# Kernel optimization log

Measured on AMD Instinct MI355X. Metric: run time of the kernel, lower is better.

The kernel has to match this reference:

```python
import jax, jax.numpy as jnp
import numpy as np

N_NODES = 50000
N_EDGES = 1000000
F_IN, HID, N_CLS, HEADS = 128, 16, 40, 8
NEG_SLOPE = 0.2


def setup_inputs() -> dict:
    key = jax.random.key(0)
    ks = jax.random.split(key, 12)
    x = jax.random.normal(ks[0], (N_NODES, F_IN), dtype=jnp.float32)
    edge_index = jax.random.randint(ks[1], (2, N_EDGES), 0, N_NODES, dtype=jnp.int32)
    s1 = 1.0 / np.sqrt(F_IN)
    s2 = 1.0 / np.sqrt(HID)
    return {
        "x": x,
        "edge_index": edge_index,
        # conv1: heads=8, out=HID, concat=False (mean over heads)
        "W1": jax.random.normal(ks[2], (F_IN, HEADS * HID), dtype=jnp.float32) * s1,
        "att_src1": jax.random.normal(ks[3], (HEADS, HID), dtype=jnp.float32) * s2,
        "att_dst1": jax.random.normal(ks[4], (HEADS, HID), dtype=jnp.float32) * s2,
        "b1": jnp.zeros((HID,), dtype=jnp.float32),
        # conv2: heads=1, out=N_CLS
        "W2": jax.random.normal(ks[5], (HID, N_CLS), dtype=jnp.float32) * s2,
        "att_src2": jax.random.normal(ks[6], (1, N_CLS), dtype=jnp.float32),
        "att_dst2": jax.random.normal(ks[7], (1, N_CLS), dtype=jnp.float32),
        "b2": jnp.zeros((N_CLS,), dtype=jnp.float32),
    }


def _gat_conv(x, src, dst, W, att_src, att_dst, num_nodes):
    """One GATConv (PyG semantics, eval mode). Returns [N, H, C]."""
    H, C = att_src.shape
    h = (x @ W).reshape(-1, H, C)                       # [N, H, C]
    a_s = (h * att_src[None]).sum(-1)                   # [N, H]
    a_d = (h * att_dst[None]).sum(-1)                   # [N, H]
    e = jax.nn.leaky_relu(a_s[src] + a_d[dst], NEG_SLOPE)  # [E, H]
    # segment softmax over edges grouped by destination node
    m = jax.ops.segment_max(e, dst, num_segments=num_nodes)     # [N, H]
    ex = jnp.exp(e - m[dst])
    denom = jax.ops.segment_sum(ex, dst, num_segments=num_nodes)
    alpha = ex / (denom[dst] + 1e-16)                   # [E, H]
    msg = h[src] * alpha[:, :, None]                    # [E, H, C]
    return jax.ops.segment_sum(msg, dst, num_segments=num_nodes)  # [N, H, C]


def reference(x, edge_index, W1, att_src1, att_dst1, b1, W2, att_src2, att_dst2, b2):
    n = x.shape[0]
    loops = jnp.arange(n, dtype=edge_index.dtype)
    src = jnp.concatenate([edge_index[0], loops])
    dst = jnp.concatenate([edge_index[1], loops])

    # conv1: concat=False -> mean over heads, then bias; then ELU
    h1 = _gat_conv(x, src, dst, W1, att_src1, att_dst1, n).mean(axis=1) + b1
    h1 = jax.nn.elu(h1)
    # dropout is identity in eval mode

    # conv2: heads=1, concat (trivial) -> squeeze head dim, add bias
    h2 = _gat_conv(h1, src, dst, W2, att_src2, att_dst2, n)[:, 0, :] + b2
    return jax.nn.log_softmax(h2, axis=1)
```

## Files before the change

kernel.cpp:

```cpp
#include <hip/hip_runtime.h>
#include <hip/hip_fp16.h>
#include <math.h>

#define N_NODES 50000
#define N_EDGES 1000000
#define F_IN 128
#define HID 16
#define N_CLS 40
#define HEADS 8
#define ET (N_EDGES + N_NODES)
#define XB ((N_NODES + 63) / 64)
#define NBK 196
#define NSB 256
#define ECH ((ET + NSB - 1) / NSB)

__device__ __forceinline__ void fma4(float4& acc, float s, const float4& v) {
  acc.x += s * v.x;
  acc.y += s * v.y;
  acc.z += s * v.z;
  acc.w += s * v.w;
}

__device__ __forceinline__ float dot4(float4 a, float4 b) {
  return a.x * b.x + a.y * b.y + a.z * b.z + a.w * b.w;
}

__device__ __forceinline__ unsigned encf(float f) {
  unsigned b = __float_as_uint(f);
  return (b & 0x80000000u) ? ~b : (b | 0x80000000u);
}
__device__ __forceinline__ float decf(unsigned k) {
  unsigned b = (k & 0x80000000u) ? (k ^ 0x80000000u) : ~k;
  return __uint_as_float(b);
}


__global__ __launch_bounds__(256, 4) void k_xform1(
    const float* __restrict__ x, const float* __restrict__ W1,
    const float* __restrict__ att_s, const float* __restrict__ att_d,
    __half* __restrict__ h1, float* __restrict__ as1, float* __restrict__ ad1,
    unsigned* __restrict__ enc1) {
  __shared__ float4 xlds[64 * 9];
  __shared__ float4 wlds[32 * 33];
  __shared__ unsigned encl[8];
  int t = threadIdx.x;
  if (t < 8) encl[t] = 0u;
  int tx = t & 15, ty = t >> 4;
  int base = blockIdx.x * 64;
  const float4* x4 = (const float4*)x;
  const float4* W4 = (const float4*)W1;

  float4 accA[4], accB[4];
#pragma unroll
  for (int n = 0; n < 4; n++) {
    accA[n] = {0.f, 0.f, 0.f, 0.f};
    accB[n] = {0.f, 0.f, 0.f, 0.f};
  }
  int n0 = ty * 4;

  for (int kb = 0; kb < 4; kb++) {
    __syncthreads();
    {
      int i = t;
      int n = i >> 3, q = i & 7;
      int gn = base + n;
      float4 v = {0.f, 0.f, 0.f, 0.f};
      if (gn < N_NODES) v = x4[(size_t)gn * 32 + kb * 8 + q];
      xlds[n * 9 + q] = v;
      i += 256;
      n = i >> 3; q = i & 7;
      gn = base + n;
      float4 v2 = {0.f, 0.f, 0.f, 0.f};
      if (gn < N_NODES) v2 = x4[(size_t)gn * 32 + kb * 8 + q];
      xlds[n * 9 + q] = v2;
    }
#pragma unroll
    for (int u = 0; u < 4; u++) {
      int i = t + u * 256;
      int r = i >> 5, q = i & 31;
      wlds[r * 33 + q] = W4[(size_t)(kb * 32 + r) * 32 + q];
    }
    __syncthreads();
#pragma unroll
    for (int kk = 0; kk < 8; kk++) {
      float4 xv0 = xlds[(n0 + 0) * 9 + kk];
      float4 xv1 = xlds[(n0 + 1) * 9 + kk];
      float4 xv2 = xlds[(n0 + 2) * 9 + kk];
      float4 xv3 = xlds[(n0 + 3) * 9 + kk];
#pragma unroll
      for (int j = 0; j < 4; j++) {
        float4 wA = wlds[(kk * 4 + j) * 33 + tx];
        float4 wB = wlds[(kk * 4 + j) * 33 + tx + 16];
        float s0 = (j == 0) ? xv0.x : (j == 1) ? xv0.y : (j == 2) ? xv0.z : xv0.w;
        float s1 = (j == 0) ? xv1.x : (j == 1) ? xv1.y : (j == 2) ? xv1.z : xv1.w;
        float s2 = (j == 0) ? xv2.x : (j == 1) ? xv2.y : (j == 2) ? xv2.z : xv2.w;
        float s3 = (j == 0) ? xv3.x : (j == 1) ? xv3.y : (j == 2) ? xv3.z : xv3.w;
        fma4(accA[0], s0, wA); fma4(accB[0], s0, wB);
        fma4(accA[1], s1, wA); fma4(accB[1], s1, wB);
        fma4(accA[2], s2, wA); fma4(accB[2], s2, wB);
        fma4(accA[3], s3, wA); fma4(accB[3], s3, wB);
      }
    }
  }

  int c4 = tx * 4;
  float4 asA = *(const float4*)(att_s + c4);
  float4 asB = *(const float4*)(att_s + 64 + c4);
  float4 adA = *(const float4*)(att_d + c4);
  float4 adB = *(const float4*)(att_d + 64 + c4);
  float mxA = -1e30f, mxB = -1e30f;
#pragma unroll
  for (int n = 0; n < 4; n++) {
    int gn = base + n0 + n;
    float psA = dot4(accA[n], asA);
    float psB = dot4(accB[n], asB);
    float pdA = dot4(accA[n], adA);
    float pdB = dot4(accB[n], adB);
    psA += __shfl_xor(psA, 1); psA += __shfl_xor(psA, 2);
    psB += __shfl_xor(psB, 1); psB += __shfl_xor(psB, 2);
    pdA += __shfl_xor(pdA, 1); pdA += __shfl_xor(pdA, 2);
    pdB += __shfl_xor(pdB, 1); pdB += __shfl_xor(pdB, 2);
    if (gn < N_NODES) {
      uint2 pkA, pkB;
      __half2* phA = (__half2*)&pkA;
      __half2* phB = (__half2*)&pkB;
      phA[0] = __floats2half2_rn(accA[n].x, accA[n].y);
      phA[1] = __floats2half2_rn(accA[n].z, accA[n].w);
      phB[0] = __floats2half2_rn(accB[n].x, accB[n].y);
      phB[1] = __floats2half2_rn(accB[n].z, accB[n].w);
      *(uint2*)(h1 + (size_t)gn * 128 + c4) = pkA;
      *(uint2*)(h1 + (size_t)gn * 128 + 64 + c4) = pkB;
      mxA = fmaxf(mxA, psA);
      mxB = fmaxf(mxB, psB);
      if ((tx & 3) == 0) {
        as1[gn * 8 + (tx >> 2)] = psA;
        as1[gn * 8 + 4 + (tx >> 2)] = psB;
        ad1[gn * 8 + (tx >> 2)] = pdA;
        ad1[gn * 8 + 4 + (tx >> 2)] = pdB;
      }
    }
  }
  if ((tx & 3) == 0) {
    atomicMax(&encl[tx >> 2], encf(mxA));
    atomicMax(&encl[4 + (tx >> 2)], encf(mxB));
  }
  __syncthreads();
  if (t < 8) atomicMax(&enc1[t], encl[t]);
}


__global__ __launch_bounds__(256) void k_rxA(const int* __restrict__ ei,
                                             int* __restrict__ bcnt) {
  __shared__ int cnt[NBK];
  int t = threadIdx.x, blk = blockIdx.x;
  if (t < NBK) cnt[t] = 0;
  __syncthreads();
  int lo = blk * ECH + t;
  int hi = min((blk + 1) * ECH, ET);
  for (int i = lo; i < hi; i += 256) {
    int d = (i < N_EDGES) ? ei[N_EDGES + i] : (i - N_EDGES);
    atomicAdd(&cnt[d >> 8], 1);
  }
  __syncthreads();
  if (t < NBK) bcnt[t * NSB + blk] = cnt[t];
}


__global__ __launch_bounds__(256) void k_rxScanB(const int* __restrict__ bcnt,
                                                 int* __restrict__ boffs,
                                                 int* __restrict__ btot) {
  __shared__ int s[256];
  int b = blockIdx.x, t = threadIdx.x;
  int v0 = bcnt[b * NSB + t];
  s[t] = v0;
  __syncthreads();
  for (int off = 1; off < 256; off <<= 1) {
    int v = (t >= off) ? s[t - off] : 0;
    __syncthreads();
    s[t] += v;
    __syncthreads();
  }
  boffs[b * NSB + t] = s[t] - v0;
  if (t == 255) btot[b] = s[255];
}


__global__ __launch_bounds__(256) void k_rxTot(const int* __restrict__ btot,
                                               int* __restrict__ bstart,
                                               int* __restrict__ start,
                                               const unsigned* __restrict__ enc1,
                                               float* __restrict__ fmax1) {
  __shared__ int s[256];
  int t = threadIdx.x;
  int v0 = (t < NBK) ? btot[t] : 0;
  s[t] = v0;
  __syncthreads();
  for (int off = 1; off < 256; off <<= 1) {
    int v = (t >= off) ? s[t - off] : 0;
    __syncthreads();
    s[t] += v;
    __syncthreads();
  }
  if (t < NBK) bstart[t] = s[t] - v0;
  if (t == 0) start[N_NODES] = ET;
  if (t < 8) fmax1[t] = decf(enc1[t]);
}


__global__ __launch_bounds__(256) void k_rxScat(const int* __restrict__ ei,
                                                const int* __restrict__ bstart,
                                                const int* __restrict__ boffs,
                                                int2* __restrict__ eb) {
  __shared__ int cur[NBK];
  int t = threadIdx.x, blk = blockIdx.x;
  if (t < NBK) cur[t] = bstart[t] + boffs[t * NSB + blk];
  __syncthreads();
  int lo = blk * ECH + t;
  int hi = min((blk + 1) * ECH, ET);
  for (int i = lo; i < hi; i += 256) {
    int s, d;
    if (i < N_EDGES) { s = ei[i]; d = ei[N_EDGES + i]; }
    else { s = i - N_EDGES; d = s; }
    int pos = atomicAdd(&cur[d >> 8], 1);
    eb[pos] = make_int2(s, d);
  }
}


__global__ __launch_bounds__(256) void k_rxB(const int2* __restrict__ eb,
                                             const int* __restrict__ bstart,
                                             int* __restrict__ start,
                                             int* __restrict__ esrc) {
  __shared__ int dcnt[256], lst[256], ssc[256];
  __shared__ int esl[8192];
  int t = threadIdx.x, b = blockIdx.x;
  int nlo = b * 256;
  int nn = min(256, N_NODES - nlo);
  int e0 = bstart[b];
  int e1 = (b == NBK - 1) ? ET : bstart[b + 1];
  int cnt = e1 - e0;
  dcnt[t] = 0;
  __syncthreads();
  for (int e = t; e < cnt; e += 256) atomicAdd(&dcnt[eb[e0 + e].y & 255], 1);
  __syncthreads();
  int v0 = dcnt[t];
  ssc[t] = v0;
  __syncthreads();
  for (int off = 1; off < 256; off <<= 1) {
    int v = (t >= off) ? ssc[t - off] : 0;
    __syncthreads();
    ssc[t] += v;
    __syncthreads();
  }
  lst[t] = ssc[t] - v0;
  if (t < nn) start[nlo + t] = e0 + lst[t];
  dcnt[t] = lst[t];
  __syncthreads();
  for (int e = t; e < cnt; e += 256) {
    int2 p = eb[e0 + e];
    int pos = atomicAdd(&dcnt[p.y & 255], 1);
    esl[pos] = p.x;
  }
  __syncthreads();
  for (int e = t; e < cnt; e += 256) esrc[e0 + e] = esl[e];
}


__global__ __launch_bounds__(256) void k_agg1(
    const __half* __restrict__ h1, const float* __restrict__ as1,
    const float* __restrict__ ad1, const int* __restrict__ start,
    const int* __restrict__ esrc, const float* __restrict__ b1,
    const float* __restrict__ W2, const float* __restrict__ att_s2,
    const float* __restrict__ att_d2, const float* __restrict__ fmax1,
    __half* __restrict__ h2, float* __restrict__ as2, float* __restrict__ ad2) {
  __shared__ __align__(16) __half2 p_t[4][4 * 164];
  __shared__ __align__(16) int s_off[4][4][20];
  __shared__ float w2s[16 * 40];
  int t = threadIdx.x;
  for (int i = t; i < 640; i += 256) w2s[i] = W2[i];
  __syncthreads();

  int wave = t >> 6, lane = t & 63;
  int g = lane >> 4, li = lane & 15;
  int d = blockIdx.x * 16 + wave * 4 + g;
  int s0 = start[d];
  int deg = start[d + 1] - s0;

  int dm = deg;
  dm = max(dm, __shfl_xor(dm, 16));
  dm = max(dm, __shfl_xor(dm, 32));

  float4 av0 = *(const float4*)(ad1 + d * 8);
  float4 av1 = *(const float4*)(ad1 + d * 8 + 4);
  float ad_[8] = {av0.x, av0.y, av0.z, av0.w, av1.x, av1.y, av1.z, av1.w};
  float c_[8];
#pragma unroll
  for (int h = 0; h < 8; h++) {
    float e = fmax1[h] + ad_[h];
    c_[h] = e > 0.f ? e : 0.2f * e;
  }

  float den = 0.f;
  float accf[8];
#pragma unroll
  for (int k = 0; k < 8; k++) accf[k] = 0.f;

  int hsel = li >> 1;
  const char* h1l = (const char*)(h1 + li * 8);
  __half2* ptw = &p_t[wave][g * 164];
  const int* so = &s_off[wave][g][0];

  for (int be = 0; be < dm; be += 16) {
    int cnt = deg - be;
    bool act = li < cnt;
    int s = 0;
    if (act) s = esrc[s0 + be + li];
    s_off[wave][g][li] = act ? (s << 8) : 0;
    float4 p0 = {0.f, 0.f, 0.f, 0.f}, p1 = {0.f, 0.f, 0.f, 0.f};
    if (act) {
      p0 = *(const float4*)(as1 + (size_t)s * 8);
      p1 = *(const float4*)(as1 + (size_t)s * 8 + 4);
    }
    float ev[8] = {p0.x, p0.y, p0.z, p0.w, p1.x, p1.y, p1.z, p1.w};
#pragma unroll
    for (int h = 0; h < 8; h++) {
      float v = ev[h] + ad_[h];
      v = v > 0.f ? v : 0.2f * v;
      float pv = act ? __expf(v - c_[h]) : 0.f;
      __half hp = __float2half(pv);
      ptw[h * 20 + li] = __half2{hp, hp};
    }
    asm volatile("s_waitcnt lgkmcnt(0)" ::: "memory");

    int cm = min(dm - be, 16);
    const __half2* pt = ptw + hsel * 20;
    __half2 a0 = __floats2half2_rn(0.f, 0.f);
    __half2 a1 = __floats2half2_rn(0.f, 0.f);
    __half2 a2 = __floats2half2_rn(0.f, 0.f);
    __half2 a3 = __floats2half2_rn(0.f, 0.f);
    for (int e = 0; e < cm; e += 8) {
      int4 s4 = *(const int4*)&so[e];
      int4 s8 = *(const int4*)&so[e + 4];
      uint4 pwA = *(const uint4*)&pt[e];
      uint4 pwB = *(const uint4*)&pt[e + 4];
      const __half2* ppA = (const __half2*)&pwA;
      const __half2* ppB = (const __half2*)&pwB;
      uint4 hA = *(const uint4*)(h1l + (unsigned)s4.x);
      uint4 hB = *(const uint4*)(h1l + (unsigned)s4.y);
      uint4 hC = *(const uint4*)(h1l + (unsigned)s4.z);
      uint4 hD = *(const uint4*)(h1l + (unsigned)s4.w);
      uint4 hE = *(const uint4*)(h1l + (unsigned)s8.x);
      uint4 hF = *(const uint4*)(h1l + (unsigned)s8.y);
      uint4 hG = *(const uint4*)(h1l + (unsigned)s8.z);
      uint4 hH = *(const uint4*)(h1l + (unsigned)s8.w);
      const __half2* vA = (const __half2*)&hA;
      const __half2* vB = (const __half2*)&hB;
      const __half2* vC = (const __half2*)&hC;
      const __half2* vD = (const __half2*)&hD;
      const __half2* vE = (const __half2*)&hE;
      const __half2* vF = (const __half2*)&hF;
      const __half2* vG = (const __half2*)&hG;
      const __half2* vH = (const __half2*)&hH;
      a0 = __hfma2(vA[0], ppA[0], a0); a1 = __hfma2(vA[1], ppA[0], a1);
      a2 = __hfma2(vA[2], ppA[0], a2); a3 = __hfma2(vA[3], ppA[0], a3);
      a0 = __hfma2(vB[0], ppA[1], a0); a1 = __hfma2(vB[1], ppA[1], a1);
      a2 = __hfma2(vB[2], ppA[1], a2); a3 = __hfma2(vB[3], ppA[1], a3);
      a0 = __hfma2(vC[0], ppA[2], a0); a1 = __hfma2(vC[1], ppA[2], a1);
      a2 = __hfma2(vC[2], ppA[2], a2); a3 = __hfma2(vC[3], ppA[2], a3);
      a0 = __hfma2(vD[0], ppA[3], a0); a1 = __hfma2(vD[1], ppA[3], a1);
      a2 = __hfma2(vD[2], ppA[3], a2); a3 = __hfma2(vD[3], ppA[3], a3);
      a0 = __hfma2(vE[0], ppB[0], a0); a1 = __hfma2(vE[1], ppB[0], a1);
      a2 = __hfma2(vE[2], ppB[0], a2); a3 = __hfma2(vE[3], ppB[0], a3);
      a0 = __hfma2(vF[0], ppB[1], a0); a1 = __hfma2(vF[1], ppB[1], a1);
      a2 = __hfma2(vF[2], ppB[1], a2); a3 = __hfma2(vF[3], ppB[1], a3);
      a0 = __hfma2(vG[0], ppB[2], a0); a1 = __hfma2(vG[1], ppB[2], a1);
      a2 = __hfma2(vG[2], ppB[2], a2); a3 = __hfma2(vG[3], ppB[2], a3);
      a0 = __hfma2(vH[0], ppB[3], a0); a1 = __hfma2(vH[1], ppB[3], a1);
      a2 = __hfma2(vH[2], ppB[3], a2); a3 = __hfma2(vH[3], ppB[3], a3);
      den += __low2float(ppA[0]) + __low2float(ppA[1]) +
             __low2float(ppA[2]) + __low2float(ppA[3]) +
             __low2float(ppB[0]) + __low2float(ppB[1]) +
             __low2float(ppB[2]) + __low2float(ppB[3]);
    }
    float2 f0 = __half22float2(a0), f1 = __half22float2(a1);
    float2 f2 = __half22float2(a2), f3 = __half22float2(a3);
    accf[0] += f0.x; accf[1] += f0.y; accf[2] += f1.x; accf[3] += f1.y;
    accf[4] += f2.x; accf[5] += f2.y; accf[6] += f3.x; accf[7] += f3.y;
    asm volatile("s_waitcnt lgkmcnt(0)" ::: "memory");
  }

  float sc = 0.125f / den;
#pragma unroll
  for (int k = 0; k < 8; k++) accf[k] *= sc;
#pragma unroll
  for (int off = 2; off <= 8; off <<= 1) {
#pragma unroll
    for (int k = 0; k < 8; k++) accf[k] += __shfl_xor(accf[k], off);
  }
  int jb = (li & 1) * 8;
  float4 b1a = *(const float4*)(b1 + jb);
  float4 b1b = *(const float4*)(b1 + jb + 4);
  float bv[8] = {b1a.x, b1a.y, b1a.z, b1a.w, b1b.x, b1b.y, b1b.z, b1b.w};
  float r[8];
#pragma unroll
  for (int k = 0; k < 8; k++) {
    float v = accf[k] + bv[k];
    r[k] = v > 0.f ? v : __expf(v) - 1.f;
  }
  float ro[8];
#pragma unroll
  for (int k = 0; k < 8; k++) ro[k] = __shfl_xor(r[k], 1);

  float o0 = 0.f, o1 = 0.f, o2 = 0.f;
  bool has2 = li < 8;
#pragma unroll
  for (int k = 0; k < 16; k++) {
    float rk;
    if (k < 8) rk = (li & 1) ? ro[k] : r[k];
    else       rk = (li & 1) ? r[k - 8] : ro[k - 8];
    o0 = fmaf(rk, w2s[k * 40 + li], o0);
    o1 = fmaf(rk, w2s[k * 40 + li + 16], o1);
    if (has2) o2 = fmaf(rk, w2s[k * 40 + li + 32], o2);
  }
  __half* h2r = h2 + d * 40;
  h2r[li] = __float2half(o0);
  h2r[li + 16] = __float2half(o1);
  if (has2) h2r[li + 32] = __float2half(o2);

  float sv = o0 * att_s2[li] + o1 * att_s2[li + 16];
  float dv = o0 * att_d2[li] + o1 * att_d2[li + 16];
  if (has2) {
    sv = fmaf(o2, att_s2[li + 32], sv);
    dv = fmaf(o2, att_d2[li + 32], dv);
  }
#pragma unroll
  for (int off = 1; off <= 8; off <<= 1) {
    sv += __shfl_xor(sv, off);
    dv += __shfl_xor(dv, off);
  }
  if (li == 0) { as2[d] = sv; ad2[d] = dv; }
}


__global__ __launch_bounds__(256) void k_maxas2(const float* __restrict__ as2,
                                                unsigned* __restrict__ enc) {
  int t = blockIdx.x * 256 + threadIdx.x;
  float mx = -1e30f;
  for (int r = t; r < N_NODES; r += 16384) mx = fmaxf(mx, as2[r]);
#pragma unroll
  for (int off = 32; off; off >>= 1) mx = fmaxf(mx, __shfl_xor(mx, off));
  if ((threadIdx.x & 63) == 0) atomicMax(enc, encf(mx));
}


__global__ __launch_bounds__(256) void k_agg2(
    const __half* __restrict__ h2, const float* __restrict__ as2,
    const float* __restrict__ ad2, const int* __restrict__ start,
    const int* __restrict__ esrc, const float* __restrict__ b2,
    const unsigned* __restrict__ as2maxEnc, float* __restrict__ out) {
  __shared__ __align__(16) float p_l[4][64];
  __shared__ __align__(16) int s_l[4][64];
  int wave = threadIdx.x >> 6, lane = threadIdx.x & 63;
  int d = blockIdx.x * 4 + wave;
  if (d >= N_NODES) return;
  int s0 = start[d];
  int deg = start[d + 1] - s0;
  float adv = ad2[d];
  float cm = decf(as2maxEnc[0]) + adv;
  cm = cm > 0.f ? cm : 0.2f * cm;

  int cp = lane % 20;
  int es = lane / 20;
  const char* h2b = (const char*)h2 + cp * 4;

  float den = 0.f, acc0 = 0.f, acc1 = 0.f;
  for (int be = 0; be < deg; be += 64) {
    int cnt = min(64, deg - be);
    if (lane < cnt) {
      int s = esrc[s0 + be + lane];
      s_l[wave][lane] = s * 80;
      float e = as2[s] + adv;
      e = e > 0.f ? e : 0.2f * e;
      float p = __expf(e - cm);
      den += p;
      p_l[wave][lane] = p;
    }
    asm volatile("s_waitcnt lgkmcnt(0)" ::: "memory");
    if (es < 3) {
      int i = 0;
      for (; i + 5 < cnt; i += 6) {
        int eA = i + es, eB = i + 3 + es;
        int sbA = s_l[wave][eA], sbB = s_l[wave][eB];
        float pA = p_l[wave][eA], pB = p_l[wave][eB];
        __half2 hvA = *(const __half2*)(h2b + (unsigned)sbA);
        __half2 hvB = *(const __half2*)(h2b + (unsigned)sbB);
        acc0 = fmaf(__half2float(hvA.x), pA, acc0);
        acc1 = fmaf(__half2float(hvA.y), pA, acc1);
        acc0 = fmaf(__half2float(hvB.x), pB, acc0);
        acc1 = fmaf(__half2float(hvB.y), pB, acc1);
      }
      for (; i < cnt; i += 3) {
        int e = i + es;
        if (e < cnt) {
          int sb = s_l[wave][e];
          float p = p_l[wave][e];
          __half2 hv = *(const __half2*)(h2b + (unsigned)sb);
          acc0 = fmaf(__half2float(hv.x), p, acc0);
          acc1 = fmaf(__half2float(hv.y), p, acc1);
        }
      }
    }
    asm volatile("s_waitcnt lgkmcnt(0)" ::: "memory");
  }
#pragma unroll
  for (int off = 32; off; off >>= 1) den += __shfl_xor(den, off);
  float iv = 1.f / den;

  acc0 += __shfl(acc0, lane + 20) + __shfl(acc0, lane + 40);
  acc1 += __shfl(acc1, lane + 20) + __shfl(acc1, lane + 40);
  float va = __shfl(acc0, lane >> 1);
  float vb = __shfl(acc1, lane >> 1);
  float v = (lane & 1) ? vb : va;
  v = (lane < N_CLS) ? v * iv + b2[lane] : -1e30f;

  float mx = v;
#pragma unroll
  for (int off = 32; off; off >>= 1) mx = fmaxf(mx, __shfl_xor(mx, off));
  float ex = (lane < N_CLS) ? __expf(v - mx) : 0.f;
  float sm = ex;
#pragma unroll
  for (int off = 32; off; off >>= 1) sm += __shfl_xor(sm, off);
  float lse = logf(sm);
  if (lane < N_CLS) out[d * N_CLS + lane] = (v - mx) - lse;
}


extern "C" void kernel_launch(void* const* d_in, const int* in_sizes, int n_in,
                              void* d_out, int out_size, void* d_ws, size_t ws_size,
                              hipStream_t stream) {
  const float* x    = (const float*)d_in[0];
  const int*   ei   = (const int*)d_in[1];
  const float* W1   = (const float*)d_in[2];
  const float* as1w = (const float*)d_in[3];
  const float* ad1w = (const float*)d_in[4];
  const float* b1   = (const float*)d_in[5];
  const float* W2   = (const float*)d_in[6];
  const float* as2w = (const float*)d_in[7];
  const float* ad2w = (const float*)d_in[8];
  const float* b2   = (const float*)d_in[9];
  float* out = (float*)d_out;

  char* ws = (char*)d_ws;
  size_t off = 0;
  auto alloc = [&](size_t bytes) -> void* {
    void* p = ws + off;
    off += (bytes + 255) & ~(size_t)255;
    return p;
  };
  __half* h1   = (__half*)alloc((size_t)N_NODES * 128 * 2);
  float* as1   = (float*)alloc((size_t)N_NODES * 8 * 4);
  float* ad1   = (float*)alloc((size_t)N_NODES * 8 * 4);
  __half* h2   = (__half*)alloc((size_t)N_NODES * 40 * 2);
  float* as2   = (float*)alloc((size_t)N_NODES * 4);
  float* ad2   = (float*)alloc((size_t)N_NODES * 4);
  unsigned* maxenc = (unsigned*)alloc(256);
  int* start   = (int*)alloc((size_t)(N_NODES + 1) * 4);
  int* esrc    = (int*)alloc((size_t)ET * 4);
  int2* eb     = (int2*)alloc((size_t)ET * 8);
  int* bcnt    = (int*)alloc((size_t)NBK * NSB * 4);
  int* boffs   = (int*)alloc((size_t)NBK * NSB * 4);
  int* btot    = (int*)alloc((size_t)NBK * 4);
  int* bstart  = (int*)alloc((size_t)NBK * 4);
  float* fmax1 = (float*)alloc(32);

  (void)hipMemsetAsync(maxenc, 0, 256, stream);

  k_xform1<<<XB, 256, 0, stream>>>(x, W1, as1w, ad1w, h1, as1, ad1, maxenc);
  k_rxA<<<NSB, 256, 0, stream>>>(ei, bcnt);
  k_rxScanB<<<NBK, 256, 0, stream>>>(bcnt, boffs, btot);
  k_rxTot<<<1, 256, 0, stream>>>(btot, bstart, start, maxenc, fmax1);
  k_rxScat<<<NSB, 256, 0, stream>>>(ei, bstart, boffs, eb);
  k_rxB<<<NBK, 256, 0, stream>>>(eb, bstart, start, esrc);

  k_agg1<<<N_NODES / 16, 256, 0, stream>>>(h1, as1, ad1, start, esrc, b1,
                                           W2, as2w, ad2w, fmax1,
                                           h2, as2, ad2);
  k_maxas2<<<64, 256, 0, stream>>>(as2, maxenc + 8);
  k_agg2<<<(N_NODES + 3) / 4, 256, 0, stream>>>(h2, as2, ad2, start, esrc, b2,
                                                maxenc + 8, out);
}
```

Before: 158.0 us.

## Aggregate 16-wide hidden features in conv2 and apply W2 after aggregation

Layer two is reordered by linearity: the edge aggregation now runs over the 16-wide ELU output h1 instead of the 40-wide projected h2, and the W2 projection is applied once per node after aggregation. The attention logits for conv2 come from precomputed vectors W2·att_src2 and W2·att_dst2, built in the small scan kernel. This cuts gathered bytes per edge from 80 to 32 and removes the per-node matmul from k_agg1. In exchange it adds a per-node 16x40 matvec with shuffles in k_agg2, and fp16 rounding now happens before the projection instead of after it.

After: 156.7 us. No clear change (-0.8%).

```diff
diff --git a/kernel.cpp b/kernel.cpp
--- a/kernel.cpp
+++ b/kernel.cpp
@@ -165,7 +165,6 @@
   if (t < NBK) bcnt[t * NSB + blk] = cnt[t];
 }
 
-
 __global__ __launch_bounds__(256) void k_rxScanB(const int* __restrict__ bcnt,
                                                  int* __restrict__ boffs,
                                                  int* __restrict__ btot) {
@@ -189,7 +188,12 @@
                                                int* __restrict__ bstart,
                                                int* __restrict__ start,
                                                const unsigned* __restrict__ enc1,
-                                               float* __restrict__ fmax1) {
+                                               float* __restrict__ fmax1,
+                                               const float* __restrict__ W2,
+                                               const float* __restrict__ att_s2,
+                                               const float* __restrict__ att_d2,
+                                               float* __restrict__ va,
+                                               float* __restrict__ vd) {
   __shared__ int s[256];
   int t = threadIdx.x;
   int v0 = (t < NBK) ? btot[t] : 0;
@@ -204,8 +208,17 @@
   if (t < NBK) bstart[t] = s[t] - v0;
   if (t == 0) start[N_NODES] = ET;
   if (t < 8) fmax1[t] = decf(enc1[t]);
-}
-
+  if (t < 16) {
+    float a = 0.f, dd = 0.f;
+    for (int j = 0; j < N_CLS; j++) {
+      float w = W2[t * N_CLS + j];
+      a = fmaf(w, att_s2[j], a);
+      dd = fmaf(w, att_d2[j], dd);
+    }
+    va[t] = a;
+    vd[t] = dd;
+  }
+}
 
 __global__ __launch_bounds__(256) void k_rxScat(const int* __restrict__ ei,
                                                 const int* __restrict__ bstart,
@@ -225,7 +238,6 @@
     eb[pos] = make_int2(s, d);
   }
 }
-
 
 __global__ __launch_bounds__(256) void k_rxB(const int2* __restrict__ eb,
                                              const int* __restrict__ bstart,
@@ -270,15 +282,12 @@
     const __half* __restrict__ h1, const float* __restrict__ as1,
     const float* __restrict__ ad1, const int* __restrict__ start,
     const int* __restrict__ esrc, const float* __restrict__ b1,
-    const float* __restrict__ W2, const float* __restrict__ att_s2,
-    const float* __restrict__ att_d2, const float* __restrict__ fmax1,
-    __half* __restrict__ h2, float* __restrict__ as2, float* __restrict__ ad2) {
+    const float* __restrict__ va, const float* __restrict__ vd,
+    const float* __restrict__ fmax1,
+    __half* __restrict__ h1o, float* __restrict__ as2, float* __restrict__ ad2) {
   __shared__ __align__(16) __half2 p_t[4][4 * 164];
   __shared__ __align__(16) int s_off[4][4][20];
-  __shared__ float w2s[16 * 40];
   int t = threadIdx.x;
-  for (int i = t; i < 640; i += 256) w2s[i] = W2[i];
-  __syncthreads();
 
   int wave = t >> 6, lane = t & 63;
   int g = lane >> 4, li = lane & 15;
@@ -407,37 +416,26 @@
     float v = accf[k] + bv[k];
     r[k] = v > 0.f ? v : __expf(v) - 1.f;
   }
-  float ro[8];
-#pragma unroll
-  for (int k = 0; k < 8; k++) ro[k] = __shfl_xor(r[k], 1);
-
-  float o0 = 0.f, o1 = 0.f, o2 = 0.f;
-  bool has2 = li < 8;
-#pragma unroll
-  for (int k = 0; k < 16; k++) {
-    float rk;
-    if (k < 8) rk = (li & 1) ? ro[k] : r[k];
-    else       rk = (li & 1) ? r[k - 8] : ro[k - 8];
-    o0 = fmaf(rk, w2s[k * 40 + li], o0);
-    o1 = fmaf(rk, w2s[k * 40 + li + 16], o1);
-    if (has2) o2 = fmaf(rk, w2s[k * 40 + li + 32], o2);
-  }
-  __half* h2r = h2 + d * 40;
-  h2r[li] = __float2half(o0);
-  h2r[li + 16] = __float2half(o1);
-  if (has2) h2r[li + 32] = __float2half(o2);
-
-  float sv = o0 * att_s2[li] + o1 * att_s2[li + 16];
-  float dv = o0 * att_d2[li] + o1 * att_d2[li + 16];
-  if (has2) {
-    sv = fmaf(o2, att_s2[li + 32], sv);
-    dv = fmaf(o2, att_d2[li + 32], dv);
-  }
-#pragma unroll
-  for (int off = 1; off <= 8; off <<= 1) {
-    sv += __shfl_xor(sv, off);
-    dv += __shfl_xor(dv, off);
-  }
+
+  if (li < 2) {
+    uint4 pk;
+    __half2* ph = (__half2*)&pk;
+    ph[0] = __floats2half2_rn(r[0], r[1]);
+    ph[1] = __floats2half2_rn(r[2], r[3]);
+    ph[2] = __floats2half2_rn(r[4], r[5]);
+    ph[3] = __floats2half2_rn(r[6], r[7]);
+    *(uint4*)(h1o + (size_t)d * 16 + li * 8) = pk;
+  }
+  float4 vaA = *(const float4*)(va + jb);
+  float4 vaB = *(const float4*)(va + jb + 4);
+  float4 vdA = *(const float4*)(vd + jb);
+  float4 vdB = *(const float4*)(vd + jb + 4);
+  float sv = r[0] * vaA.x + r[1] * vaA.y + r[2] * vaA.z + r[3] * vaA.w +
+             r[4] * vaB.x + r[5] * vaB.y + r[6] * vaB.z + r[7] * vaB.w;
+  float dv = r[0] * vdA.x + r[1] * vdA.y + r[2] * vdA.z + r[3] * vdA.w +
+             r[4] * vdB.x + r[5] * vdB.y + r[6] * vdB.z + r[7] * vdB.w;
+  sv += __shfl_xor(sv, 1);
+  dv += __shfl_xor(dv, 1);
   if (li == 0) { as2[d] = sv; ad2[d] = dv; }
 }
 
@@ -454,13 +452,19 @@
 
 
 __global__ __launch_bounds__(256) void k_agg2(
-    const __half* __restrict__ h2, const float* __restrict__ as2,
+    const __half* __restrict__ h1o, const float* __restrict__ as2,
     const float* __restrict__ ad2, const int* __restrict__ start,
     const int* __restrict__ esrc, const float* __restrict__ b2,
-    const unsigned* __restrict__ as2maxEnc, float* __restrict__ out) {
+    const float* __restrict__ W2, const unsigned* __restrict__ as2maxEnc,
+    float* __restrict__ out) {
   __shared__ __align__(16) float p_l[4][64];
   __shared__ __align__(16) int s_l[4][64];
-  int wave = threadIdx.x >> 6, lane = threadIdx.x & 63;
+  __shared__ float w2s[16 * 40];
+  int t = threadIdx.x;
+  for (int i = t; i < 640; i += 256) w2s[i] = W2[i];
+  __syncthreads();
+
+  int wave = t >> 6, lane = t & 63;
   int d = blockIdx.x * 4 + wave;
   if (d >= N_NODES) return;
   int s0 = start[d];
@@ -469,16 +473,16 @@
   float cm = decf(as2maxEnc[0]) + adv;
   cm = cm > 0.f ? cm : 0.2f * cm;
 
-  int cp = lane % 20;
-  int es = lane / 20;
-  const char* h2b = (const char*)h2 + cp * 4;
+  int cp = lane & 7;
+  int es = lane >> 3;
+  const char* hb = (const char*)h1o + cp * 4;
 
   float den = 0.f, acc0 = 0.f, acc1 = 0.f;
   for (int be = 0; be < deg; be += 64) {
     int cnt = min(64, deg - be);
     if (lane < cnt) {
       int s = esrc[s0 + be + lane];
-      s_l[wave][lane] = s * 80;
+      s_l[wave][lane] = s * 32;
       float e = as2[s] + adv;
       e = e > 0.f ? e : 0.2f * e;
       float p = __expf(e - cm);
@@ -486,29 +490,23 @@
       p_l[wave][lane] = p;
     }
     asm volatile("s_waitcnt lgkmcnt(0)" ::: "memory");
-    if (es < 3) {
-      int i = 0;
-      for (; i + 5 < cnt; i += 6) {
-        int eA = i + es, eB = i + 3 + es;
-        int sbA = s_l[wave][eA], sbB = s_l[wave][eB];
-        float pA = p_l[wave][eA], pB = p_l[wave][eB];
-        __half2 hvA = *(const __half2*)(h2b + (unsigned)sbA);
-        __half2 hvB = *(const __half2*)(h2b + (unsigned)sbB);
-        acc0 = fmaf(__half2float(hvA.x), pA, acc0);
-        acc1 = fmaf(__half2float(hvA.y), pA, acc1);
-        acc0 = fmaf(__half2float(hvB.x), pB, acc0);
-        acc1 = fmaf(__half2float(hvB.y), pB, acc1);
-      }
-      for (; i < cnt; i += 3) {
-        int e = i + es;
-        if (e < cnt) {
-          int sb = s_l[wave][e];
-          float p = p_l[wave][e];
-          __half2 hv = *(const __half2*)(h2b + (unsigned)sb);
-          acc0 = fmaf(__half2float(hv.x), p, acc0);
-          acc1 = fmaf(__half2float(hv.y), p, acc1);
-        }
-      }
+    int i = es;
+    for (; i + 8 < cnt; i += 16) {
+      int sbA = s_l[wave][i], sbB = s_l[wave][i + 8];
+      float pA = p_l[wave][i], pB = p_l[wave][i + 8];
+      __half2 hvA = *(const __half2*)(hb + (unsigned)sbA);
+      __half2 hvB = *(const __half2*)(hb + (unsigned)sbB);
+      acc0 = fmaf(__half2float(hvA.x), pA, acc0);
+      acc1 = fmaf(__half2float(hvA.y), pA, acc1);
+      acc0 = fmaf(__half2float(hvB.x), pB, acc0);
+      acc1 = fmaf(__half2float(hvB.y), pB, acc1);
+    }
+    if (i < cnt) {
+      int sb = s_l[wave][i];
+      float p = p_l[wave][i];
+      __half2 hv = *(const __half2*)(hb + (unsigned)sb);
+      acc0 = fmaf(__half2float(hv.x), p, acc0);
+      acc1 = fmaf(__half2float(hv.y), p, acc1);
     }
     asm volatile("s_waitcnt lgkmcnt(0)" ::: "memory");
   }
@@ -516,12 +514,19 @@
   for (int off = 32; off; off >>= 1) den += __shfl_xor(den, off);
   float iv = 1.f / den;
 
-  acc0 += __shfl(acc0, lane + 20) + __shfl(acc0, lane + 40);
-  acc1 += __shfl(acc1, lane + 20) + __shfl(acc1, lane + 40);
-  float va = __shfl(acc0, lane >> 1);
-  float vb = __shfl(acc1, lane >> 1);
-  float v = (lane & 1) ? vb : va;
-  v = (lane < N_CLS) ? v * iv + b2[lane] : -1e30f;
+  acc0 += __shfl_xor(acc0, 8);  acc1 += __shfl_xor(acc1, 8);
+  acc0 += __shfl_xor(acc0, 16); acc1 += __shfl_xor(acc1, 16);
+  acc0 += __shfl_xor(acc0, 32); acc1 += __shfl_xor(acc1, 32);
+  float m0 = acc0 * iv, m1 = acc1 * iv;
+
+  float v = 0.f;
+#pragma unroll
+  for (int k = 0; k < 16; k++) {
+    float ms = (k & 1) ? m1 : m0;
+    float mk = __shfl(ms, k >> 1);
+    if (lane < N_CLS) v = fmaf(mk, w2s[k * 40 + lane], v);
+  }
+  v = (lane < N_CLS) ? v + b2[lane] : -1e30f;
 
   float mx = v;
 #pragma unroll
@@ -560,7 +565,7 @@
   __half* h1   = (__half*)alloc((size_t)N_NODES * 128 * 2);
   float* as1   = (float*)alloc((size_t)N_NODES * 8 * 4);
   float* ad1   = (float*)alloc((size_t)N_NODES * 8 * 4);
-  __half* h2   = (__half*)alloc((size_t)N_NODES * 40 * 2);
+  __half* h1o  = (__half*)alloc((size_t)N_NODES * 16 * 2);
   float* as2   = (float*)alloc((size_t)N_NODES * 4);
   float* ad2   = (float*)alloc((size_t)N_NODES * 4);
   unsigned* maxenc = (unsigned*)alloc(256);
@@ -572,20 +577,22 @@
   int* btot    = (int*)alloc((size_t)NBK * 4);
   int* bstart  = (int*)alloc((size_t)NBK * 4);
   float* fmax1 = (float*)alloc(32);
+  float* va    = (float*)alloc(64);
+  float* vd    = (float*)alloc(64);
 
   (void)hipMemsetAsync(maxenc, 0, 256, stream);
 
   k_xform1<<<XB, 256, 0, stream>>>(x, W1, as1w, ad1w, h1, as1, ad1, maxenc);
   k_rxA<<<NSB, 256, 0, stream>>>(ei, bcnt);
   k_rxScanB<<<NBK, 256, 0, stream>>>(bcnt, boffs, btot);
-  k_rxTot<<<1, 256, 0, stream>>>(btot, bstart, start, maxenc, fmax1);
+  k_rxTot<<<1, 256, 0, stream>>>(btot, bstart, start, maxenc, fmax1,
+                                 W2, as2w, ad2w, va, vd);
   k_rxScat<<<NSB, 256, 0, stream>>>(ei, bstart, boffs, eb);
   k_rxB<<<NBK, 256, 0, stream>>>(eb, bstart, start, esrc);
 
   k_agg1<<<N_NODES / 16, 256, 0, stream>>>(h1, as1, ad1, start, esrc, b1,
-                                           W2, as2w, ad2w, fmax1,
-                                           h2, as2, ad2);
+                                           va, vd, fmax1, h1o, as2, ad2);
   k_maxas2<<<64, 256, 0, stream>>>(as2, maxenc + 8);
-  k_agg2<<<(N_NODES + 3) / 4, 256, 0, stream>>>(h2, as2, ad2, start, esrc, b2,
-                                                maxenc + 8, out);
-}
+  k_agg2<<<(N_NODES + 3) / 4, 256, 0, stream>>>(h1o, as2, ad2, start, esrc, b2,
+                                                W2, maxenc + 8, out);
+}
```
